# Optimization experiments

Measured on AMD Instinct MI355X. Metric: run time of the kernel, lower is better.

## Reference

```python
import jax, jax.numpy as jnp
import numpy as np

CHANNELS = 256

def setup_inputs() -> dict:
    key = jax.random.key(0)
    ks = jax.random.split(key, 7)
    B, C, N = 4, CHANNELS, 4096
    scale = 1.0 / np.sqrt(C)
    x = jax.random.normal(ks[0], (B, C, N), dtype=jnp.float32)
    Wq = jax.random.normal(ks[1], (C, C), dtype=jnp.float32) * scale
    bq = jax.random.normal(ks[2], (C,), dtype=jnp.float32) * 0.01
    Wk = jax.random.normal(ks[3], (C, C), dtype=jnp.float32) * scale
    bk = jax.random.normal(ks[4], (C,), dtype=jnp.float32) * 0.01
    Wv = jax.random.normal(ks[5], (C, C), dtype=jnp.float32) * scale
    bv = jax.random.normal(ks[6], (C,), dtype=jnp.float32) * 0.01
    return {"x": x, "Wq": Wq, "bq": bq, "Wk": Wk, "bk": bk, "Wv": Wv, "bv": bv}

def reference(x, Wq, bq, Wk, bk, Wv, bv):
    # x: [B, C, N]; 1x1 Conv1d == channel-mixing matmul
    C = x.shape[1]
    Q = jnp.einsum('oc,bcn->bon', Wq, x) + bq[None, :, None]   # [B, C, N]
    K = jnp.einsum('oc,bcn->bon', Wk, x) + bk[None, :, None]   # [B, C, N]
    V = jnp.einsum('oc,bcn->bon', Wv, x) + bv[None, :, None]   # [B, C, N]
    # attn[b, i, j] = softmax_j( Q[:, i]^T K[:, j] / sqrt(C) )
    scores = jnp.einsum('bci,bcj->bij', Q, K) / jnp.sqrt(jnp.asarray(C, x.dtype))
    attn = jax.nn.softmax(scores, axis=-1)                     # [B, N, N]
    context = jnp.einsum('bij,bcj->bci', attn, V)              # [B, C, N]
    return x + context
```

## Files before the change

kernel.cpp:

```cpp
#include <hip/hip_runtime.h>
#include <stdint.h>

#define B_ 4
#define C_ 256
#define N_ 4096
#define JS 4

typedef unsigned short u16;
typedef __attribute__((ext_vector_type(4))) float f32x4;
typedef __attribute__((ext_vector_type(16))) float f32x16;
typedef __attribute__((ext_vector_type(8))) short bf16x8;
typedef __attribute__((ext_vector_type(4))) int i32x4;

__device__ __forceinline__ u16 f2bf(float f) {
    uint32_t u = __float_as_uint(f);
    u += 0x7fffu + ((u >> 16) & 1u);
    return (u16)(u >> 16);
}
__device__ __forceinline__ float bf2f(u16 v) {
    uint32_t u = ((uint32_t)v) << 16;
    return __uint_as_float(u);
}
__device__ __forceinline__ uint32_t pkbf(float a, float b) {
    uint32_t ua = __float_as_uint(a) + 0x8000u;
    uint32_t ub = __float_as_uint(b) + 0x8000u;
    return (ua >> 16) | (ub & 0xffff0000u);
}

#if defined(__has_builtin)
#if __has_builtin(__builtin_amdgcn_global_load_lds)
#define HAVE_GLL 1
#endif
#endif

#ifdef HAVE_GLL
__device__ __forceinline__ void g2l16(const u16* g, u16* lbase, int lane) {
    (void)lane;
    __builtin_amdgcn_global_load_lds(
        (__attribute__((address_space(1))) void*)(uintptr_t)g,
        (__attribute__((address_space(3))) void*)lbase, 16, 0, 0);
}
#else
__device__ __forceinline__ void g2l16(const u16* g, u16* lbase, int lane) {
    *(i32x4*)(lbase + lane * 8) = *(const i32x4*)g;
}
#endif

__global__ __launch_bounds__(256) void wconv_kernel(
    const float* __restrict__ Wq, const float* __restrict__ Wk,
    const float* __restrict__ Wv, u16* __restrict__ Wb) {
    int id = blockIdx.x * 256 + threadIdx.x;
    const float* src = (id < 65536) ? Wq : ((id < 131072) ? Wk : Wv);
    Wb[id] = f2bf(src[id & 65535]);
}

__global__ __launch_bounds__(256, 2) void qkv_kernel(
    const float* __restrict__ x, const u16* __restrict__ Wb,
    const float* __restrict__ bq, const float* __restrict__ bk,
    const float* __restrict__ bv,
    u16* __restrict__ Qt, u16* __restrict__ Kt, u16* __restrict__ Vt) {
    const int XTS = 264;
    __shared__ __align__(16) u16 xT[32 * XTS];

    int blk = blockIdx.x;
    int n0  = (blk & 127) << 5;
    int b   = blk >> 7;
    int tid = threadIdx.x;
    int lane = tid & 63;
    int w = tid >> 6;
    int l31 = lane & 31;
    int h = lane >> 5;

    {
        int c0 = tid >> 3;
        int nq = (tid & 7) << 2;
        const float* xb = x + ((size_t)b * C_ + c0) * N_ + n0 + nq;
        #pragma unroll
        for (int p = 0; p < 8; ++p) {
            f32x4 v = *(const f32x4*)(xb + (size_t)32 * N_ * p);
            int cc = c0 + 32 * p;
            xT[(nq + 0) * XTS + cc] = f2bf(v[0]);
            xT[(nq + 1) * XTS + cc] = f2bf(v[1]);
            xT[(nq + 2) * XTS + cc] = f2bf(v[2]);
            xT[(nq + 3) * XTS + cc] = f2bf(v[3]);
        }
    }
    __syncthreads();

    bf16x8 xf[16];
    #pragma unroll
    for (int ks = 0; ks < 16; ++ks)
        xf[ks] = *(const bf16x8*)(&xT[l31 * XTS + 16 * ks + 8 * h]);

    #pragma unroll
    for (int mat = 0; mat < 2; ++mat) {
        const u16* W = Wb + mat * 65536;
        const float* bias = mat ? bk : bq;
        u16* dst = mat ? Kt : Qt;
        f32x16 acc0, acc1;
        #pragma unroll
        for (int r = 0; r < 16; ++r) { acc0[r] = 0.f; acc1[r] = 0.f; }
        const u16* wr0 = W + (size_t)(64 * w + l31) * 256 + 8 * h;
        const u16* wr1 = W + (size_t)(64 * w + 32 + l31) * 256 + 8 * h;
        #pragma unroll
        for (int ks = 0; ks < 16; ++ks) {
            bf16x8 wf0 = *(const bf16x8*)(wr0 + 16 * ks);
            bf16x8 wf1 = *(const bf16x8*)(wr1 + 16 * ks);
            acc0 = __builtin_amdgcn_mfma_f32_32x32x16_bf16(xf[ks], wf0, acc0, 0, 0, 0);
            acc1 = __builtin_amdgcn_mfma_f32_32x32x16_bf16(xf[ks], wf1, acc1, 0, 0, 0);
        }
        #pragma unroll
        for (int ot = 0; ot < 2; ++ot) {
            const f32x16& a = ot ? acc1 : acc0;
            int o = 64 * w + 32 * ot + l31;
            float bo = bias[o];
            #pragma unroll
            for (int g = 0; g < 4; ++g)
                #pragma unroll
                for (int r = 0; r < 4; ++r) {
                    int n = 8 * g + 4 * h + r;
                    int oc = mat ? ((((o >> 3) ^ n) << 3) | (o & 7)) : o;
                    dst[((size_t)b * N_ + n0 + n) * C_ + oc] = f2bf(a[4 * g + r] + bo);
                }
        }
    }

    {
        const u16* W = Wb + 2 * 65536;
        f32x16 acc0, acc1;
        #pragma unroll
        for (int r = 0; r < 16; ++r) { acc0[r] = 0.f; acc1[r] = 0.f; }
        const u16* wr0 = W + (size_t)(64 * w + l31) * 256 + 8 * h;
        const u16* wr1 = W + (size_t)(64 * w + 32 + l31) * 256 + 8 * h;
        #pragma unroll
        for (int ks = 0; ks < 16; ++ks) {
            bf16x8 wf0 = *(const bf16x8*)(wr0 + 16 * ks);
            bf16x8 wf1 = *(const bf16x8*)(wr1 + 16 * ks);
            acc0 = __builtin_amdgcn_mfma_f32_32x32x16_bf16(wf0, xf[ks], acc0, 0, 0, 0);
            acc1 = __builtin_amdgcn_mfma_f32_32x32x16_bf16(wf1, xf[ks], acc1, 0, 0, 0);
        }
        int nj = n0 + l31;
        int tb = nj & ~63;
        int local = nj & 63;
        #pragma unroll
        for (int mt = 0; mt < 2; ++mt) {
            const f32x16& a = mt ? acc1 : acc0;
            #pragma unroll
            for (int g = 0; g < 4; ++g)
                #pragma unroll
                for (int r = 0; r < 4; ++r) {
                    int o = 64 * w + 32 * mt + 8 * g + 4 * h + r;
                    int njs = tb | ((((local >> 3) ^ (o & 7)) << 3) | (local & 7));
                    Vt[((size_t)b * C_ + o) * N_ + njs] = f2bf(a[4 * g + r] + bv[o]);
                }
        }
    }
}

__device__ __forceinline__ void stage64(const u16* Kb, const u16* Vb, int j0,
                                        u16* ksd, u16* vsd, int w, int lane) {
    const u16* kg = Kb + (size_t)(j0 + 8 * w) * C_ + lane * 8;
    u16* kdb = ksd + 8 * w * 256;
    #pragma unroll
    for (int rr = 0; rr < 4; ++rr)
        g2l16(kg + rr * 512, kdb + rr * 512, lane);
    const u16* vg = Vb + (size_t)(32 * w + (lane >> 3)) * N_ + j0 + (lane & 7) * 8;
    u16* vdb = vsd + 32 * w * 64;
    #pragma unroll
    for (int rr = 0; rr < 4; ++rr)
        g2l16(vg + (size_t)8 * rr * N_, vdb + rr * 512, lane);
}

__global__ __launch_bounds__(512, 2) void attn_kernel(
    const u16* __restrict__ Qt, const u16* __restrict__ Kt,
    const u16* __restrict__ Vt, u16* __restrict__ Op,
    float* __restrict__ lArr) {
    __shared__ __align__(16) u16 Ksh[2 * 64 * 256];
    __shared__ __align__(16) u16 Vsh[2 * 256 * 64];

    int blk = blockIdx.x;
    int it = blk & 15;
    int b  = (blk >> 4) & 3;
    int s  = blk >> 6;
    int i0 = it << 8;
    int tid = threadIdx.x;
    int lane = tid & 63;
    int w = tid >> 6;
    int l31 = lane & 31;
    int h = lane >> 5;

    bf16x8 qf[16];
    {
        const u16* qrow = Qt + ((size_t)b * N_ + i0 + 32 * w + l31) * C_ + 8 * h;
        #pragma unroll
        for (int ks = 0; ks < 16; ++ks) qf[ks] = *(const bf16x8*)(qrow + 16 * ks);
    }

    f32x16 oacc[8];
    #pragma unroll
    for (int mt = 0; mt < 8; ++mt)
        #pragma unroll
        for (int r = 0; r < 16; ++r) oacc[mt][r] = 0.f;
    float l_run = 0.f;

    const float sconst = 0.0625f * 1.44269504088896340736f;
    const u16* Kb = Kt + (size_t)b * N_ * C_;
    const u16* Vb = Vt + (size_t)b * C_ * N_;
    int jbase = s * (N_ / JS);

    stage64(Kb, Vb, jbase, Ksh, Vsh, w, lane);
    __syncthreads();

    for (int jt = 0; jt < N_ / (64 * JS); ++jt) {
        int cur = jt & 1;
        const u16* ks_ = Ksh + cur * 64 * 256;
        const u16* vs_ = Vsh + cur * 256 * 64;

        if (jt + 1 < N_ / (64 * JS))
            stage64(Kb, Vb, jbase + (jt + 1) * 64,
                    Ksh + (cur ^ 1) * 64 * 256, Vsh + (cur ^ 1) * 256 * 64, w, lane);

        f32x16 st0, st1;
        #pragma unroll
        for (int r = 0; r < 16; ++r) { st0[r] = 0.f; st1[r] = 0.f; }
        #pragma unroll
        for (int ks = 0; ks < 16; ++ks) {
            int kc = ((2 * ks + h) ^ l31) << 3;
            bf16x8 kf0 = *(const bf16x8*)(ks_ + l31 * 256 + kc);
            bf16x8 kf1 = *(const bf16x8*)(ks_ + (32 + l31) * 256 + kc);
            st0 = __builtin_amdgcn_mfma_f32_32x32x16_bf16(kf0, qf[ks], st0, 0, 0, 0);
            st1 = __builtin_amdgcn_mfma_f32_32x32x16_bf16(kf1, qf[ks], st1, 0, 0, 0);
        }

        float psum = 0.f;
        uint32_t pd[16];
        #pragma unroll
        for (int u = 0; u < 8; ++u) {
            const f32x16& stv = (u < 4) ? st0 : st1;
            int g = u & 3;
            #pragma unroll
            for (int d = 0; d < 2; ++d) {
                float p0 = exp2f(stv[4 * g + 2 * d + 0] * sconst);
                float p1 = exp2f(stv[4 * g + 2 * d + 1] * sconst);
                psum += p0 + p1;
                pd[u * 2 + d] = pkbf(p0, p1);
            }
        }
        psum += __shfl_xor(psum, 32);
        l_run += psum;

        bf16x8 pf[4];
        #pragma unroll
        for (int ks2 = 0; ks2 < 4; ++ks2) {
            uint32_t oA0 = pd[4 * ks2 + 0], oA1 = pd[4 * ks2 + 1];
            uint32_t oB0 = pd[4 * ks2 + 2], oB1 = pd[4 * ks2 + 3];
            uint32_t sn0 = h ? oA0 : oB0, sn1 = h ? oA1 : oB1;
            uint32_t rc0 = (uint32_t)__shfl_xor((int)sn0, 32);
            uint32_t rc1 = (uint32_t)__shfl_xor((int)sn1, 32);
            uint32_t ow0 = h ? oB0 : oA0, ow1 = h ? oB1 : oA1;
            i32x4 fr;
            fr[0] = (int)(h ? rc0 : ow0);
            fr[1] = (int)(h ? rc1 : ow1);
            fr[2] = (int)(h ? ow0 : rc0);
            fr[3] = (int)(h ? ow1 : rc1);
            pf[ks2] = *(bf16x8*)&fr;
        }

        #pragma unroll
        for (int ks2 = 0; ks2 < 4; ++ks2) {
            int vc = ((2 * ks2 + h) ^ (l31 & 7)) << 3;
            #pragma unroll
            for (int mt = 0; mt < 8; ++mt) {
                bf16x8 vf = *(const bf16x8*)(vs_ + (32 * mt + l31) * 64 + vc);
                oacc[mt] = __builtin_amdgcn_mfma_f32_32x32x16_bf16(vf, pf[ks2], oacc[mt], 0, 0, 0);
            }
        }
        __syncthreads();
    }

    int i = i0 + 32 * w + l31;
    u16* ob = Op + ((size_t)(s * B_ + b) * C_) * N_ + i;
    #pragma unroll
    for (int mt = 0; mt < 8; ++mt)
        #pragma unroll
        for (int g = 0; g < 4; ++g)
            #pragma unroll
            for (int r = 0; r < 4; ++r) {
                int c = 32 * mt + 8 * g + r + 4 * h;
                ob[(size_t)c * N_] = f2bf(oacc[mt][4 * g + r]);
            }
    if (h == 0) lArr[(size_t)(s * B_ + b) * N_ + i] = l_run;
}

__global__ __launch_bounds__(256) void merge_kernel(
    const float* __restrict__ x, const u16* __restrict__ Op,
    const float* __restrict__ lArr, float* __restrict__ out) {
    int blk = blockIdx.x;
    int ch = blk & 1;
    int ib = (blk >> 1) & 63;
    int b  = blk >> 7;
    int i  = ib * 64 + (threadIdx.x & 63);
    int csub = threadIdx.x >> 6;

    float L = 0.f;
    #pragma unroll
    for (int s = 0; s < JS; ++s) L += lArr[(size_t)(s * B_ + b) * N_ + i];
    float rL = 1.0f / L;

    for (int cc = 0; cc < 32; ++cc) {
        int c = ch * 128 + csub * 32 + cc;
        size_t xi = ((size_t)b * C_ + c) * N_ + i;
        float acc = 0.f;
        #pragma unroll
        for (int s = 0; s < JS; ++s)
            acc += bf2f(Op[((size_t)(s * B_ + b) * C_ + c) * N_ + i]);
        out[xi] = fmaf(acc, rL, x[xi]);
    }
}

extern "C" void kernel_launch(void* const* d_in, const int* in_sizes, int n_in,
                              void* d_out, int out_size, void* d_ws, size_t ws_size,
                              hipStream_t stream) {
    const float* x  = (const float*)d_in[0];
    const float* Wq = (const float*)d_in[1];
    const float* bq = (const float*)d_in[2];
    const float* Wk = (const float*)d_in[3];
    const float* bk = (const float*)d_in[4];
    const float* Wv = (const float*)d_in[5];
    const float* bv = (const float*)d_in[6];
    float* out = (float*)d_out;

    u16* Wb = (u16*)d_ws;
    u16* Qt = Wb + 3 * 65536;
    u16* Kt = Qt + (size_t)B_ * N_ * C_;
    u16* Vt = Kt + (size_t)B_ * N_ * C_;
    u16* Op = Vt + (size_t)B_ * N_ * C_;
    float* lArr = (float*)(Op + (size_t)JS * B_ * C_ * N_);

    wconv_kernel<<<768, 256, 0, stream>>>(Wq, Wk, Wv, Wb);
    qkv_kernel<<<512, 256, 0, stream>>>(x, Wb, bq, bk, bv, Qt, Kt, Vt);
    attn_kernel<<<256, 512, 0, stream>>>(Qt, Kt, Vt, Op, lArr);
    merge_kernel<<<512, 256, 0, stream>>>(x, Op, lArr, out);
}
```

Baseline: 205.3 us.

## Split score tiles to overlap exp with PV MFMAs and vectorize merge

```diff
diff --git a/kernel.cpp b/kernel.cpp
--- a/kernel.cpp
+++ b/kernel.cpp
@@ -25,6 +25,18 @@
     uint32_t ua = __float_as_uint(a) + 0x8000u;
     uint32_t ub = __float_as_uint(b) + 0x8000u;
     return (ua >> 16) | (ub & 0xffff0000u);
+}
+
+__device__ __forceinline__ float fexp2(float x) {
+#if defined(__has_builtin)
+#if __has_builtin(__builtin_amdgcn_exp2f)
+    return __builtin_amdgcn_exp2f(x);
+#else
+    return exp2f(x);
+#endif
+#else
+    return exp2f(x);
+#endif
 }
 
 #if defined(__has_builtin)
@@ -207,53 +219,60 @@
     const u16* Kb = Kt + (size_t)b * N_ * C_;
     const u16* Vb = Vt + (size_t)b * C_ * N_;
     int jbase = s * (N_ / JS);
+    const int NT = N_ / (64 * JS);
 
     stage64(Kb, Vb, jbase, Ksh, Vsh, w, lane);
     __syncthreads();
 
-    for (int jt = 0; jt < N_ / (64 * JS); ++jt) {
+    for (int jt = 0; jt < NT; ++jt) {
         int cur = jt & 1;
         const u16* ks_ = Ksh + cur * 64 * 256;
         const u16* vs_ = Vsh + cur * 256 * 64;
 
-        if (jt + 1 < N_ / (64 * JS))
+        if (jt + 1 < NT)
             stage64(Kb, Vb, jbase + (jt + 1) * 64,
                     Ksh + (cur ^ 1) * 64 * 256, Vsh + (cur ^ 1) * 256 * 64, w, lane);
 
-        f32x16 st0, st1;
-        #pragma unroll
-        for (int r = 0; r < 16; ++r) { st0[r] = 0.f; st1[r] = 0.f; }
+        f32x16 st0;
+        #pragma unroll
+        for (int r = 0; r < 16; ++r) st0[r] = 0.f;
+        __builtin_amdgcn_s_setprio(1);
         #pragma unroll
         for (int ks = 0; ks < 16; ++ks) {
             int kc = ((2 * ks + h) ^ l31) << 3;
             bf16x8 kf0 = *(const bf16x8*)(ks_ + l31 * 256 + kc);
+            st0 = __builtin_amdgcn_mfma_f32_32x32x16_bf16(kf0, qf[ks], st0, 0, 0, 0);
+        }
+        __builtin_amdgcn_s_setprio(0);
+
+        f32x16 st1;
+        #pragma unroll
+        for (int r = 0; r < 16; ++r) st1[r] = 0.f;
+        __builtin_amdgcn_s_setprio(1);
+        #pragma unroll
+        for (int ks = 0; ks < 16; ++ks) {
+            int kc = ((2 * ks + h) ^ l31) << 3;
             bf16x8 kf1 = *(const bf16x8*)(ks_ + (32 + l31) * 256 + kc);
-            st0 = __builtin_amdgcn_mfma_f32_32x32x16_bf16(kf0, qf[ks], st0, 0, 0, 0);
             st1 = __builtin_amdgcn_mfma_f32_32x32x16_bf16(kf1, qf[ks], st1, 0, 0, 0);
         }
+        __builtin_amdgcn_s_setprio(0);
 
         float psum = 0.f;
-        uint32_t pd[16];
-        #pragma unroll
-        for (int u = 0; u < 8; ++u) {
-            const f32x16& stv = (u < 4) ? st0 : st1;
-            int g = u & 3;
+        uint32_t pd0[8];
+        #pragma unroll
+        for (int g = 0; g < 4; ++g)
             #pragma unroll
             for (int d = 0; d < 2; ++d) {
-                float p0 = exp2f(stv[4 * g + 2 * d + 0] * sconst);
-                float p1 = exp2f(stv[4 * g + 2 * d + 1] * sconst);
+                float p0 = fexp2(st0[4 * g + 2 * d + 0] * sconst);
+                float p1 = fexp2(st0[4 * g + 2 * d + 1] * sconst);
                 psum += p0 + p1;
-                pd[u * 2 + d] = pkbf(p0, p1);
+                pd0[g * 2 + d] = pkbf(p0, p1);
             }
-        }
-        psum += __shfl_xor(psum, 32);
-        l_run += psum;
-
-        bf16x8 pf[4];
-        #pragma unroll
-        for (int ks2 = 0; ks2 < 4; ++ks2) {
-            uint32_t oA0 = pd[4 * ks2 + 0], oA1 = pd[4 * ks2 + 1];
-            uint32_t oB0 = pd[4 * ks2 + 2], oB1 = pd[4 * ks2 + 3];
+        bf16x8 pf0[2];
+        #pragma unroll
+        for (int k2 = 0; k2 < 2; ++k2) {
+            uint32_t oA0 = pd0[4 * k2 + 0], oA1 = pd0[4 * k2 + 1];
+            uint32_t oB0 = pd0[4 * k2 + 2], oB1 = pd0[4 * k2 + 3];
             uint32_t sn0 = h ? oA0 : oB0, sn1 = h ? oA1 : oB1;
             uint32_t rc0 = (uint32_t)__shfl_xor((int)sn0, 32);
             uint32_t rc1 = (uint32_t)__shfl_xor((int)sn1, 32);
@@ -263,18 +282,62 @@
             fr[1] = (int)(h ? rc1 : ow1);
             fr[2] = (int)(h ? ow0 : rc0);
             fr[3] = (int)(h ? ow1 : rc1);
-            pf[ks2] = *(bf16x8*)&fr;
-        }
-
-        #pragma unroll
-        for (int ks2 = 0; ks2 < 4; ++ks2) {
-            int vc = ((2 * ks2 + h) ^ (l31 & 7)) << 3;
+            pf0[k2] = *(bf16x8*)&fr;
+        }
+
+        __builtin_amdgcn_s_setprio(1);
+        #pragma unroll
+        for (int k2 = 0; k2 < 2; ++k2) {
+            int vc = ((2 * k2 + h) ^ (l31 & 7)) << 3;
             #pragma unroll
             for (int mt = 0; mt < 8; ++mt) {
                 bf16x8 vf = *(const bf16x8*)(vs_ + (32 * mt + l31) * 64 + vc);
-                oacc[mt] = __builtin_amdgcn_mfma_f32_32x32x16_bf16(vf, pf[ks2], oacc[mt], 0, 0, 0);
+                oacc[mt] = __builtin_amdgcn_mfma_f32_32x32x16_bf16(vf, pf0[k2], oacc[mt], 0, 0, 0);
             }
         }
+        __builtin_amdgcn_s_setprio(0);
+
+        uint32_t pd1[8];
+        #pragma unroll
+        for (int g = 0; g < 4; ++g)
+            #pragma unroll
+            for (int d = 0; d < 2; ++d) {
+                float p0 = fexp2(st1[4 * g + 2 * d + 0] * sconst);
+                float p1 = fexp2(st1[4 * g + 2 * d + 1] * sconst);
+                psum += p0 + p1;
+                pd1[g * 2 + d] = pkbf(p0, p1);
+            }
+        bf16x8 pf1[2];
+        #pragma unroll
+        for (int k2 = 0; k2 < 2; ++k2) {
+            uint32_t oA0 = pd1[4 * k2 + 0], oA1 = pd1[4 * k2 + 1];
+            uint32_t oB0 = pd1[4 * k2 + 2], oB1 = pd1[4 * k2 + 3];
+            uint32_t sn0 = h ? oA0 : oB0, sn1 = h ? oA1 : oB1;
+            uint32_t rc0 = (uint32_t)__shfl_xor((int)sn0, 32);
+            uint32_t rc1 = (uint32_t)__shfl_xor((int)sn1, 32);
+            uint32_t ow0 = h ? oB0 : oA0, ow1 = h ? oB1 : oA1;
+            i32x4 fr;
+            fr[0] = (int)(h ? rc0 : ow0);
+            fr[1] = (int)(h ? rc1 : ow1);
+            fr[2] = (int)(h ? ow0 : rc0);
+            fr[3] = (int)(h ? ow1 : rc1);
+            pf1[k2] = *(bf16x8*)&fr;
+        }
+        psum += __shfl_xor(psum, 32);
+        l_run += psum;
+
+        __builtin_amdgcn_s_setprio(1);
+        #pragma unroll
+        for (int k2 = 0; k2 < 2; ++k2) {
+            int vc = ((2 * (k2 + 2) + h) ^ (l31 & 7)) << 3;
+            #pragma unroll
+            for (int mt = 0; mt < 8; ++mt) {
+                bf16x8 vf = *(const bf16x8*)(vs_ + (32 * mt + l31) * 64 + vc);
+                oacc[mt] = __builtin_amdgcn_mfma_f32_32x32x16_bf16(vf, pf1[k2], oacc[mt], 0, 0, 0);
+            }
+        }
+        __builtin_amdgcn_s_setprio(0);
+
         __syncthreads();
     }
 
@@ -295,26 +358,49 @@
 __global__ __launch_bounds__(256) void merge_kernel(
     const float* __restrict__ x, const u16* __restrict__ Op,
     const float* __restrict__ lArr, float* __restrict__ out) {
+    __shared__ float rLs[64];
     int blk = blockIdx.x;
-    int ch = blk & 1;
-    int ib = (blk >> 1) & 63;
-    int b  = blk >> 7;
-    int i  = ib * 64 + (threadIdx.x & 63);
-    int csub = threadIdx.x >> 6;
-
-    float L = 0.f;
-    #pragma unroll
-    for (int s = 0; s < JS; ++s) L += lArr[(size_t)(s * B_ + b) * N_ + i];
-    float rL = 1.0f / L;
-
-    for (int cc = 0; cc < 32; ++cc) {
-        int c = ch * 128 + csub * 32 + cc;
-        size_t xi = ((size_t)b * C_ + c) * N_ + i;
-        float acc = 0.f;
-        #pragma unroll
-        for (int s = 0; s < JS; ++s)
-            acc += bf2f(Op[((size_t)(s * B_ + b) * C_ + c) * N_ + i]);
-        out[xi] = fmaf(acc, rL, x[xi]);
+    int cg = blk & 3;
+    int ic = (blk >> 2) & 63;
+    int b  = blk >> 8;
+    int i0 = ic << 6;
+    int tid = threadIdx.x;
+
+    if (tid < 64) {
+        float L = 0.f;
+        #pragma unroll
+        for (int s = 0; s < JS; ++s) L += lArr[(size_t)(s * B_ + b) * N_ + i0 + tid];
+        rLs[tid] = 1.0f / L;
+    }
+    __syncthreads();
+
+    int i8 = (tid & 7) << 3;
+    int c  = (cg << 6) + ((tid >> 3) << 1);
+    f32x4 rl0 = *(const f32x4*)&rLs[i8];
+    f32x4 rl1 = *(const f32x4*)&rLs[i8 + 4];
+
+    #pragma unroll
+    for (int cc = 0; cc < 2; ++cc) {
+        size_t xoff = ((size_t)b * C_ + c + cc) * N_ + i0 + i8;
+        float acc[8];
+        #pragma unroll
+        for (int e = 0; e < 8; ++e) acc[e] = 0.f;
+        #pragma unroll
+        for (int s = 0; s < JS; ++s) {
+            bf16x8 o = *(const bf16x8*)&Op[((size_t)(s * B_ + b) * C_ + c + cc) * N_ + i0 + i8];
+            #pragma unroll
+            for (int e = 0; e < 8; ++e) acc[e] += bf2f((u16)o[e]);
+        }
+        f32x4 xv0 = *(const f32x4*)&x[xoff];
+        f32x4 xv1 = *(const f32x4*)&x[xoff + 4];
+        f32x4 o0, o1;
+        #pragma unroll
+        for (int e = 0; e < 4; ++e) {
+            o0[e] = fmaf(acc[e], rl0[e], xv0[e]);
+            o1[e] = fmaf(acc[e + 4], rl1[e], xv1[e]);
+        }
+        *(f32x4*)&out[xoff] = o0;
+        *(f32x4*)&out[xoff + 4] = o1;
     }
 }
 
@@ -340,5 +426,5 @@
     wconv_kernel<<<768, 256, 0, stream>>>(Wq, Wk, Wv, Wb);
     qkv_kernel<<<512, 256, 0, stream>>>(x, Wb, bq, bk, bv, Qt, Kt, Vt);
     attn_kernel<<<256, 512, 0, stream>>>(Qt, Kt, Vt, Op, lArr);
-    merge_kernel<<<512, 256, 0, stream>>>(x, Op, lArr, out);
-}
+    merge_kernel<<<1024, 256, 0, stream>>>(x, Op, lArr, out);
+}
```

New measurement: 413.6 us. 101% more time.
